# Kernel tuning notes

Measured on AMD Instinct MI355X. Metric: run time of the kernel, lower is better.

## Reference

```python
import jax, jax.numpy as jnp
import numpy as np

MARGIN = 0.5
THRESH = 0.1
B = 8192


def setup_inputs() -> dict:
    key = jax.random.key(0)
    k1, k2 = jax.random.split(key)
    predictions = jax.random.normal(k1, (B,), dtype=jnp.float32)
    targets = jax.random.uniform(k2, (B,), dtype=jnp.float32)
    return {"predictions": predictions, "targets": targets}


def _sample_masked(mask, key):
    # Uniform random choice among True entries of each row of mask [B, B].
    u = jax.random.uniform(key, mask.shape, dtype=jnp.float32)
    scores = jnp.where(mask, u, -jnp.inf)
    return jnp.argmax(scores, axis=1)  # [B] int


def reference(predictions, targets):
    preds = predictions.reshape(-1)  # handles [B] or [B,1]
    # target_diffs[i, j] = targets[i] - targets[j]
    diffs = targets[:, None] - targets[None, :]          # [B, B]
    pos_mask = diffs < -THRESH                           # j strictly better than i
    neg_mask = diffs > THRESH                            # j strictly worse than i

    key = jax.random.key(42)
    kp, kn = jax.random.split(key)
    pos_idx = _sample_masked(pos_mask, kp)               # [B]
    neg_idx = _sample_masked(neg_mask, kn)               # [B]

    valid = jnp.any(pos_mask, axis=1) & jnp.any(neg_mask, axis=1)  # [B]
    per_anchor = jnp.maximum(MARGIN - (preds[pos_idx] - preds[neg_idx]), 0.0)
    num_triplets = jnp.sum(valid.astype(jnp.float32))
    loss_sum = jnp.sum(jnp.where(valid, per_anchor, 0.0))
    loss = jnp.where(num_triplets > 0, loss_sum / jnp.maximum(num_triplets, 1.0), 0.0)
    return loss
```

## Files before the change

kernel.cpp:

```cpp
#include <hip/hip_runtime.h>
#include <stdint.h>


#define B 8192
#define K 1024

struct TFOut { uint32_t a, b; };

__host__ __device__ constexpr uint32_t rotl32(uint32_t x, int r) {
    return (x << r) | (x >> (32 - r));
}

__host__ __device__ constexpr TFOut threefry_full(uint32_t k0, uint32_t k1,
                                                  uint32_t x0, uint32_t x1) {
    const uint32_t ks2 = k0 ^ k1 ^ 0x1BD11BDAu;
    x0 += k0; x1 += k1;
    x0 += x1; x1 = rotl32(x1,13); x1 ^= x0;
    x0 += x1; x1 = rotl32(x1,15); x1 ^= x0;
    x0 += x1; x1 = rotl32(x1,26); x1 ^= x0;
    x0 += x1; x1 = rotl32(x1,6);  x1 ^= x0;
    x0 += k1; x1 += ks2 + 1u;
    x0 += x1; x1 = rotl32(x1,17); x1 ^= x0;
    x0 += x1; x1 = rotl32(x1,29); x1 ^= x0;
    x0 += x1; x1 = rotl32(x1,16); x1 ^= x0;
    x0 += x1; x1 = rotl32(x1,24); x1 ^= x0;
    x0 += ks2; x1 += k0 + 2u;
    x0 += x1; x1 = rotl32(x1,13); x1 ^= x0;
    x0 += x1; x1 = rotl32(x1,15); x1 ^= x0;
    x0 += x1; x1 = rotl32(x1,26); x1 ^= x0;
    x0 += x1; x1 = rotl32(x1,6);  x1 ^= x0;
    x0 += k0; x1 += k1 + 3u;
    x0 += x1; x1 = rotl32(x1,17); x1 ^= x0;
    x0 += x1; x1 = rotl32(x1,29); x1 ^= x0;
    x0 += x1; x1 = rotl32(x1,16); x1 ^= x0;
    x0 += x1; x1 = rotl32(x1,24); x1 ^= x0;
    x0 += k1; x1 += ks2 + 4u;
    x0 += x1; x1 = rotl32(x1,13); x1 ^= x0;
    x0 += x1; x1 = rotl32(x1,15); x1 ^= x0;
    x0 += x1; x1 = rotl32(x1,26); x1 ^= x0;
    x0 += x1; x1 = rotl32(x1,6);  x1 ^= x0;
    x0 += ks2; x1 += k0 + 5u;
    return TFOut{x0, x1};
}

constexpr TFOut KP = threefry_full(0u, 42u, 0u, 0u);
constexpr TFOut KN = threefry_full(0u, 42u, 0u, 1u);

template<uint32_t TK0, uint32_t TK1>
__device__ __forceinline__ uint32_t tf_bits(uint32_t x1) {
    constexpr uint32_t KS2 = TK0 ^ TK1 ^ 0x1BD11BDAu;
    uint32_t x0 = TK0;
#define RND(r) x0 += x1; x1 = __builtin_amdgcn_alignbit(x1, x1, 32 - (r)); x1 ^= x0;
    RND(13) RND(15) RND(26) RND(6)
    x0 += TK1; x1 += KS2 + 1u;
    RND(17) RND(29) RND(16) RND(24)
    x0 += KS2; x1 += TK0 + 2u;
    RND(13) RND(15) RND(26) RND(6)
    x0 += TK0; x1 += TK1 + 3u;
    RND(17) RND(29) RND(16) RND(24)
    x0 += TK1; x1 += KS2 + 4u;
    RND(13) RND(15) RND(26) RND(6)
    x0 += KS2; x1 += TK0 + 5u;
#undef RND
    return x0 ^ x1;
}

__device__ __forceinline__ void mrg(uint32_t& H, uint32_t& J, uint32_t h2, uint32_t j2) {
    if (h2 > H || (h2 == H && j2 < J)) { H = h2; J = j2; }
}

template<uint32_t TK0, uint32_t TK1>
__device__ __forceinline__ void scan_main(const uint16_t* __restrict__ idx,
                                          int beg, int end, int lane,
                                          uint32_t kb, uint32_t& H, uint32_t& J)
{
    uint32_t h0 = 0, h1 = 0, h2 = 0, h3 = 0;
    uint32_t j0 = 0xFFFFFFFFu, j1 = 0xFFFFFFFFu, j2 = 0xFFFFFFFFu, j3 = 0xFFFFFFFFu;
    int s = beg;
    uint32_t a = 0, b = 0, c = 0, d = 0;
    if (s + 256 <= end) {
        a = idx[s + lane];       b = idx[s + lane + 64];
        c = idx[s + lane + 128]; d = idx[s + lane + 192];
    }
    while (s + 256 <= end) {
        const int sn = s + 256;
        const uint32_t na = idx[sn + lane];
        const uint32_t nb = idx[sn + lane + 64];
        const uint32_t nc = idx[sn + lane + 128];
        const uint32_t nd = idx[sn + lane + 192];
        const uint32_t ha = tf_bits<TK0, TK1>(a + kb) >> 9;
        const uint32_t hb = tf_bits<TK0, TK1>(b + kb) >> 9;
        const uint32_t hc = tf_bits<TK0, TK1>(c + kb) >> 9;
        const uint32_t hd = tf_bits<TK0, TK1>(d + kb) >> 9;
        if (ha > h0) { h0 = ha; j0 = a; }
        if (hb > h1) { h1 = hb; j1 = b; }
        if (hc > h2) { h2 = hc; j2 = c; }
        if (hd > h3) { h3 = hd; j3 = d; }
        a = na; b = nb; c = nc; d = nd;
        s = sn;
    }
    for (int t = s + lane; t < end; t += 64) {
        const uint32_t j = idx[t];
        const uint32_t hh = tf_bits<TK0, TK1>(j + kb) >> 9;
        if (hh > h0) { h0 = hh; j0 = j; }
    }
    mrg(h0, j0, h1, j1); mrg(h2, j2, h3, j3); mrg(h0, j0, h2, j2);
    mrg(H, J, h0, j0);
}

template<uint32_t TK0, uint32_t TK1, bool NEG>
__device__ __forceinline__ void scan_bnd(const float* __restrict__ st,
                                         const uint16_t* __restrict__ idx,
                                         int beg, int end, int lane, float ti,
                                         uint32_t kb, uint32_t& H, uint32_t& J,
                                         bool& found)
{
    for (int t = beg + lane; t < end; t += 64) {
        const float tj = st[t];
        const uint32_t j = idx[t];
        const uint32_t hh = tf_bits<TK0, TK1>(j + kb) >> 9;
        const float dd = ti - tj;
        const bool ok = NEG ? (dd > 0.1f) : (dd < -0.1f);
        if (ok) {
            found = true;
            if (hh > H || (hh == H && j < J)) { H = hh; J = j; }
        }
    }
}

__global__ __launch_bounds__(1024) void sort_kernel(
    const float* __restrict__ targets,
    float* __restrict__ sorted_t, uint16_t* __restrict__ sorted_idx,
    int* __restrict__ bin_start, float* __restrict__ loss_sum,
    float* __restrict__ valid_sum, unsigned int* __restrict__ done)
{
    __shared__ int hist[K];
    __shared__ int wsum[16];
    __shared__ int cursor[K];
    const int tid = threadIdx.x;

    hist[tid] = 0;
    if (tid == 0) { *loss_sum = 0.0f; *valid_sum = 0.0f; *done = 0u; }
    __syncthreads();

    float v[B / 1024];
    int   bnum[B / 1024];
    for (int i = 0; i < B / 1024; ++i) {
        const int e = tid + i * 1024;
        v[i] = targets[e];
        int b = (int)(v[i] * (float)K);
        b = b < 0 ? 0 : (b > K - 1 ? K - 1 : b);
        bnum[i] = b;
        atomicAdd(&hist[b], 1);
    }
    __syncthreads();

    const int cnt  = hist[tid];
    const int lane = tid & 63;
    const int wv   = tid >> 6;
    int incl = cnt;
    for (int d = 1; d < 64; d <<= 1) {
        const int o = __shfl_up(incl, d, 64);
        if (lane >= d) incl += o;
    }
    if (lane == 63) wsum[wv] = incl;
    __syncthreads();
    if (tid < 16) {
        int wincl = wsum[tid];
        for (int d = 1; d < 16; d <<= 1) {
            const int o = __shfl_up(wincl, d, 64);
            if (tid >= d) wincl += o;
        }
        wsum[tid] = wincl;
    }
    __syncthreads();
    incl += (wv > 0) ? wsum[wv - 1] : 0;
    bin_start[tid + 1] = incl;
    if (tid == 0) bin_start[0] = 0;
    cursor[tid] = incl - cnt;
    __syncthreads();

    for (int i = 0; i < B / 1024; ++i) {
        const int e = tid + i * 1024;
        const int p = atomicAdd(&cursor[bnum[i]], 1);
        sorted_t[p]   = v[i];
        sorted_idx[p] = (uint16_t)e;
    }
}

__global__ __launch_bounds__(256) void rows_kernel(
    const float* __restrict__ preds, const float* __restrict__ targets,
    const float* __restrict__ sorted_t, const uint16_t* __restrict__ sorted_idx,
    const int* __restrict__ bin_start,
    float* __restrict__ loss_sum, float* __restrict__ valid_sum,
    unsigned int* __restrict__ done, float* __restrict__ out)
{
    __shared__ float sl[4], sv[4];
    const int lane = threadIdx.x & 63;
    const int wv   = threadIdx.x >> 6;
    const int row  = (blockIdx.x << 2) + wv;

    const float ti = targets[row];
    const uint32_t base = (uint32_t)row << 13;

    const float cutn = ti - 0.1f;
    int bl = (int)floorf((cutn - 1e-4f) * (float)K);
    int bh = (int)floorf((cutn + 1e-4f) * (float)K) + 1;
    bl = bl < 0 ? 0 : (bl > K ? K : bl);
    bh = bh < 0 ? 0 : (bh > K ? K : bh);
    const int un_end = bin_start[bl];
    const int cn_end = bin_start[bh];

    const float cutp = ti + 0.1f;
    int pl = (int)floorf((cutp - 1e-4f) * (float)K);
    int ph = (int)floorf((cutp + 1e-4f) * (float)K) + 1;
    pl = pl < 0 ? 0 : (pl > K ? K : pl);
    ph = ph < 0 ? 0 : (ph > K ? K : ph);
    const int cp_beg = bin_start[pl];
    const int up_beg = bin_start[ph];

    uint32_t Hn = 0, Jn = 0xFFFFFFFFu;
    bool fn = false;
    scan_main<KN.a, KN.b>(sorted_idx, 0, un_end, lane, base + KN.b, Hn, Jn);
    scan_bnd<KN.a, KN.b, true>(sorted_t, sorted_idx, un_end, cn_end, lane, ti,
                               base + KN.b, Hn, Jn, fn);
    const bool valid_n = (un_end > 0) || __any(fn);

    uint32_t Hp = 0, Jp = 0xFFFFFFFFu;
    bool fp2 = false;
    scan_main<KP.a, KP.b>(sorted_idx, up_beg, B, lane, base + KP.b, Hp, Jp);
    scan_bnd<KP.a, KP.b, false>(sorted_t, sorted_idx, cp_beg, up_beg, lane, ti,
                                base + KP.b, Hp, Jp, fp2);
    const bool valid_p = (up_beg < B) || __any(fp2);

    for (int off = 32; off > 0; off >>= 1) {
        const uint32_t ohn = __shfl_down(Hn, off, 64);
        const uint32_t ojn = __shfl_down(Jn, off, 64);
        if (ohn > Hn || (ohn == Hn && ojn < Jn)) { Hn = ohn; Jn = ojn; }
        const uint32_t ohp = __shfl_down(Hp, off, 64);
        const uint32_t ojp = __shfl_down(Jp, off, 64);
        if (ohp > Hp || (ohp == Hp && ojp < Jp)) { Hp = ohp; Jp = ojp; }
    }

    if (lane == 0) {
        float loss = 0.0f, valid = 0.0f;
        if (valid_n && valid_p) {
            const float per = 0.5f - (preds[Jp & 8191u] - preds[Jn & 8191u]);
            loss = per > 0.0f ? per : 0.0f;
            valid = 1.0f;
        }
        sl[wv] = loss; sv[wv] = valid;
    }
    __syncthreads();
    if (threadIdx.x == 0) {
        atomicAdd(loss_sum,  sl[0] + sl[1] + sl[2] + sl[3]);
        atomicAdd(valid_sum, sv[0] + sv[1] + sv[2] + sv[3]);
        __threadfence();
        const unsigned int old = atomicAdd(done, 1u);
        if (old == gridDim.x - 1u) {
            const float ls = atomicAdd(loss_sum, 0.0f);
            const float vs = atomicAdd(valid_sum, 0.0f);
            out[0] = vs > 0.0f ? ls / fmaxf(vs, 1.0f) : 0.0f;
        }
    }
}

extern "C" void kernel_launch(void* const* d_in, const int* in_sizes, int n_in,
                              void* d_out, int out_size, void* d_ws, size_t ws_size,
                              hipStream_t stream) {
    const float* preds   = (const float*)d_in[0];
    const float* targets = (const float*)d_in[1];

    float* ws = (float*)d_ws;
    float*        sorted_t   = ws;
    uint16_t*     sorted_idx = (uint16_t*)(ws + B);
    int*          bin_start  = (int*)(ws + B + B / 2 + 256);
    float*        loss_sum   = ws + B + B / 2 + 2048;
    float*        valid_sum  = loss_sum + 1;
    unsigned int* done       = (unsigned int*)(loss_sum + 2);

    sort_kernel<<<1, 1024, 0, stream>>>(targets, sorted_t, sorted_idx, bin_start,
                                        loss_sum, valid_sum, done);
    rows_kernel<<<B / 4, 256, 0, stream>>>(preds, targets, sorted_t, sorted_idx,
                                           bin_start, loss_sum, valid_sum, done,
                                           (float*)d_out);
}
```

Measured before the change: 180.4 us.

## Split single-block counting sort into multi-block histogram, scan, and scatter kernels

Replaces the one-block sort kernel with three kernels: per-block histograms over 8 blocks, a single-block scan that builds bin starts and cursors, and an 8-block scatter that uses global atomics on the cursors. The aim is to spread the histogram and scatter work across more compute units instead of one. In exchange it adds two extra kernel launches and turns the scatter's shared-memory atomics into global atomics. The per-block histograms reuse the sorted_t workspace region, which is safe because the scatter runs after the scan.

```diff
diff --git a/kernel.cpp b/kernel.cpp
--- a/kernel.cpp
+++ b/kernel.cpp
@@ -4,6 +4,7 @@
 
 #define B 8192
 #define K 1024
+#define HB 8
 
 struct TFOut { uint32_t a, b; };
 
@@ -128,62 +129,76 @@
     }
 }
 
-__global__ __launch_bounds__(1024) void sort_kernel(
-    const float* __restrict__ targets,
-    float* __restrict__ sorted_t, uint16_t* __restrict__ sorted_idx,
-    int* __restrict__ bin_start, float* __restrict__ loss_sum,
+__device__ __forceinline__ int bin_of(float v) {
+    int b = (int)(v * (float)K);
+    return b < 0 ? 0 : (b > K - 1 ? K - 1 : b);
+}
+
+__global__ __launch_bounds__(256) void hist_kernel(
+    const float* __restrict__ targets, uint16_t* __restrict__ blockHist)
+{
+    __shared__ int h[K];
+    const int tid = threadIdx.x;
+    for (int i = tid; i < K; i += 256) h[i] = 0;
+    __syncthreads();
+    const int base = blockIdx.x * (B / HB);
+    for (int i = 0; i < (B / HB) / 256; ++i)
+        atomicAdd(&h[bin_of(targets[base + tid + i * 256])], 1);
+    __syncthreads();
+    for (int i = tid; i < K; i += 256)
+        blockHist[blockIdx.x * K + i] = (uint16_t)h[i];
+}
+
+__global__ __launch_bounds__(256) void scan_kernel(
+    const uint16_t* __restrict__ blockHist, int* __restrict__ bin_start,
+    int* __restrict__ cursor, float* __restrict__ loss_sum,
     float* __restrict__ valid_sum, unsigned int* __restrict__ done)
 {
-    __shared__ int hist[K];
-    __shared__ int wsum[16];
-    __shared__ int cursor[K];
+    __shared__ int wsum[4];
     const int tid = threadIdx.x;
-
-    hist[tid] = 0;
     if (tid == 0) { *loss_sum = 0.0f; *valid_sum = 0.0f; *done = 0u; }
-    __syncthreads();
-
-    float v[B / 1024];
-    int   bnum[B / 1024];
-    for (int i = 0; i < B / 1024; ++i) {
-        const int e = tid + i * 1024;
-        v[i] = targets[e];
-        int b = (int)(v[i] * (float)K);
-        b = b < 0 ? 0 : (b > K - 1 ? K - 1 : b);
-        bnum[i] = b;
-        atomicAdd(&hist[b], 1);
-    }
-    __syncthreads();
-
-    const int cnt  = hist[tid];
-    const int lane = tid & 63;
-    const int wv   = tid >> 6;
-    int incl = cnt;
+
+    int c0 = 0, c1 = 0, c2 = 0, c3 = 0;
+    for (int s = 0; s < HB; ++s) {
+        const uint16_t* sl = blockHist + s * K + 4 * tid;
+        c0 += sl[0]; c1 += sl[1]; c2 += sl[2]; c3 += sl[3];
+    }
+    const int s4 = c0 + c1 + c2 + c3;
+
+    const int lane = tid & 63, wv = tid >> 6;
+    int incl = s4;
     for (int d = 1; d < 64; d <<= 1) {
         const int o = __shfl_up(incl, d, 64);
         if (lane >= d) incl += o;
     }
     if (lane == 63) wsum[wv] = incl;
     __syncthreads();
-    if (tid < 16) {
-        int wincl = wsum[tid];
-        for (int d = 1; d < 16; d <<= 1) {
-            const int o = __shfl_up(wincl, d, 64);
-            if (tid >= d) wincl += o;
-        }
-        wsum[tid] = wincl;
-    }
-    __syncthreads();
-    incl += (wv > 0) ? wsum[wv - 1] : 0;
-    bin_start[tid + 1] = incl;
+    int wbase = 0;
+    for (int w = 0; w < wv; ++w) wbase += wsum[w];
+    incl += wbase;
+    const int excl = incl - s4;
+
+    bin_start[4 * tid + 1] = excl + c0;
+    bin_start[4 * tid + 2] = excl + c0 + c1;
+    bin_start[4 * tid + 3] = excl + c0 + c1 + c2;
+    bin_start[4 * tid + 4] = excl + s4;
     if (tid == 0) bin_start[0] = 0;
-    cursor[tid] = incl - cnt;
-    __syncthreads();
-
-    for (int i = 0; i < B / 1024; ++i) {
-        const int e = tid + i * 1024;
-        const int p = atomicAdd(&cursor[bnum[i]], 1);
-        sorted_t[p]   = v[i];
+    cursor[4 * tid + 0] = excl;
+    cursor[4 * tid + 1] = excl + c0;
+    cursor[4 * tid + 2] = excl + c0 + c1;
+    cursor[4 * tid + 3] = excl + c0 + c1 + c2;
+}
+
+__global__ __launch_bounds__(256) void scatter_kernel(
+    const float* __restrict__ targets, int* __restrict__ cursor,
+    float* __restrict__ sorted_t, uint16_t* __restrict__ sorted_idx)
+{
+    const int base = blockIdx.x * (B / HB);
+    for (int i = 0; i < (B / HB) / 256; ++i) {
+        const int e = base + threadIdx.x + i * 256;
+        const float v = targets[e];
+        const int p = atomicAdd(&cursor[bin_of(v)], 1);
+        sorted_t[p]   = v;
         sorted_idx[p] = (uint16_t)e;
     }
 }
@@ -273,15 +288,19 @@
 
     float* ws = (float*)d_ws;
     float*        sorted_t   = ws;
+    uint16_t*     blockHist  = (uint16_t*)ws;
     uint16_t*     sorted_idx = (uint16_t*)(ws + B);
-    int*          bin_start  = (int*)(ws + B + B / 2 + 256);
-    float*        loss_sum   = ws + B + B / 2 + 2048;
-    float*        valid_sum  = loss_sum + 1;
-    unsigned int* done       = (unsigned int*)(loss_sum + 2);
-
-    sort_kernel<<<1, 1024, 0, stream>>>(targets, sorted_t, sorted_idx, bin_start,
-                                        loss_sum, valid_sum, done);
-    rows_kernel<<<B / 4, 256, 0, stream>>>(preds, targets, sorted_t, sorted_idx,
-                                           bin_start, loss_sum, valid_sum, done,
-                                           (float*)d_out);
-}
+    int*          bin_start  = (int*)(ws + 12544);
+    int*          cursor     = (int*)(ws + 13600);
+    float*        loss_sum   = ws + 14624;
+    float*        valid_sum  = ws + 14625;
+    unsigned int* done       = (unsigned int*)(ws + 14626);
+
+    hist_kernel   <<<HB,    256, 0, stream>>>(targets, blockHist);
+    scan_kernel   <<<1,     256, 0, stream>>>(blockHist, bin_start, cursor,
+                                              loss_sum, valid_sum, done);
+    scatter_kernel<<<HB,    256, 0, stream>>>(targets, cursor, sorted_t, sorted_idx);
+    rows_kernel   <<<B / 4, 256, 0, stream>>>(preds, targets, sorted_t, sorted_idx,
+                                              bin_start, loss_sum, valid_sum,
+                                              done, (float*)d_out);
+}
```

Result: no change. 178.4 us (-1.1%).
